# Kernel optimization log

Measured on AMD Instinct MI355X. Metric: run time of the kernel, lower is better.

The kernel has to match this reference:

```python
import jax, jax.numpy as jnp
import numpy as np


def setup_inputs() -> dict:
    key = jax.random.key(0)
    ks = jax.random.split(key, 4)
    B, C, H, W = 4, 256, 64, 64
    Cqk = C // 16
    x = jax.random.normal(ks[0], (B, C, H, W), dtype=jnp.float32)
    # 1x1 conv weights (fan-in scaled) and biases
    Wq = jax.random.normal(ks[1], (Cqk, C), dtype=jnp.float32) / np.sqrt(C)
    Wk = jax.random.normal(ks[2], (Cqk, C), dtype=jnp.float32) / np.sqrt(C)
    Wv = jax.random.normal(ks[3], (C, C), dtype=jnp.float32) / np.sqrt(C)
    bq = jnp.zeros((Cqk,), dtype=jnp.float32)
    bk = jnp.zeros((Cqk,), dtype=jnp.float32)
    bv = jnp.zeros((C,), dtype=jnp.float32)
    gamma = jnp.zeros((1,), dtype=jnp.float32)
    return {"x": x, "Wq": Wq, "bq": bq, "Wk": Wk, "bk": bk, "Wv": Wv, "bv": bv, "gamma": gamma}


def reference(x, Wq, bq, Wk, bk, Wv, bv, gamma):
    B, C, H, W = x.shape
    N = H * W
    xf = x.reshape(B, C, N)  # [B, C, N]
    # 1x1 convs == per-pixel channel matmuls
    q = jnp.einsum('oc,bcn->bon', Wq, xf) + bq[None, :, None]  # [B, C//16, N]
    k = jnp.einsum('oc,bcn->bon', Wk, xf) + bk[None, :, None]  # [B, C//16, N]
    v = jnp.einsum('oc,bcn->bon', Wv, xf) + bv[None, :, None]  # [B, C, N]
    # S = Q^T K : [B, N, N]
    S = jnp.einsum('bcn,bcm->bnm', q, k)
    # NOTE: original uses Softmax(dim=-2) -> normalize over the first N axis (query/row axis)
    A = jax.nn.softmax(S, axis=-2)
    # o[b,c,m] = sum_n v[b,c,n] * A[b,n,m]  (torch.bmm(proj_value, softmax(S)))
    o = jnp.einsum('bcn,bnm->bcm', v, A).reshape(B, C, H, W)
    return x + gamma[0] * o
```

## Files before the change

### kernel.cpp

```cpp
#include <hip/hip_runtime.h>
#include <hip/hip_bf16.h>


constexpr int B_  = 4;
constexpr int C_  = 256;
constexpr int N_  = 4096;
constexpr int NT  = 64;

typedef short   bf16x8  __attribute__((ext_vector_type(8)));
typedef short   short4v __attribute__((ext_vector_type(4)));
typedef unsigned short ushort8v __attribute__((ext_vector_type(8)));
typedef float   f32x4   __attribute__((ext_vector_type(4)));

__device__ __forceinline__ unsigned short f2bf(float f) {
  __hip_bfloat16 h = __float2bfloat16(f);
  return *reinterpret_cast<unsigned short*>(&h);
}

__global__ __launch_bounds__(256) void cast_w_kernel(
    const float* __restrict__ Wq, const float* __restrict__ Wk,
    const float* __restrict__ Wv, unsigned short* __restrict__ Wbf) {
  const int f = (blockIdx.x * 256 + threadIdx.x) * 8;
  const float* src;
  if (f < 4096)      src = Wq + f;
  else if (f < 8192) src = Wk + (f - 4096);
  else               src = Wv + (f - 8192);
  f32x4 a = *(const f32x4*)src;
  f32x4 c = *(const f32x4*)(src + 4);
  ushort8v o;
#pragma unroll
  for (int e = 0; e < 4; ++e) { o[e] = f2bf(a[e]); o[4 + e] = f2bf(c[e]); }
  *(ushort8v*)&Wbf[f] = o;
}

__global__ __launch_bounds__(512) void proj_fused_kernel(
    const float* __restrict__ x, const unsigned short* __restrict__ Wbf,
    const float* __restrict__ bq, const float* __restrict__ bk,
    const float* __restrict__ bv,
    unsigned short* __restrict__ qT, unsigned short* __restrict__ kT,
    unsigned short* __restrict__ vbf) {
  __shared__ __align__(16) char xsm[32768];
  const int tid = threadIdx.x;
  const int b  = blockIdx.y;
  const int n0 = blockIdx.x << 6;
  const int ln = tid & 63, w = tid >> 6;
  const int g  = ln >> 4, li = ln & 15;
  const float* xb = x + (size_t)b * C_ * N_ + n0;

#pragma unroll
  for (int pass = 0; pass < 2; ++pass) {
    const int id = pass * 512 + tid;
    const int nq = id & 15, kq = id >> 4;
    const int k = kq << 2, nn = nq << 2;
    f32x4 r0 = *(const f32x4*)&xb[(size_t)(k + 0) * N_ + nn];
    f32x4 r1 = *(const f32x4*)&xb[(size_t)(k + 1) * N_ + nn];
    f32x4 r2 = *(const f32x4*)&xb[(size_t)(k + 2) * N_ + nn];
    f32x4 r3 = *(const f32x4*)&xb[(size_t)(k + 3) * N_ + nn];
#pragma unroll
    for (int j = 0; j < 4; ++j) {
      short4v p;
      p[0] = (short)f2bf(r0[j]); p[1] = (short)f2bf(r1[j]);
      p[2] = (short)f2bf(r2[j]); p[3] = (short)f2bf(r3[j]);
      const int row = nn + j;
      const int boff = row * 512 + (((k >> 3) ^ (row & 7)) << 4) + ((k & 7) << 1);
      *(short4v*)(xsm + boff) = p;
    }
  }
  __syncthreads();

  const int nmf = (w < 2) ? 3 : 2;
  const int mfs0 = 2 * w, mfs1 = 2 * w + 1, mfs2 = 16 + w;
  f32x4 acc[3][4];
#pragma unroll
  for (int mi = 0; mi < 3; ++mi)
#pragma unroll
    for (int nf = 0; nf < 4; ++nf) acc[mi][nf] = (f32x4){0.f, 0.f, 0.f, 0.f};

  const char* wb = (const char*)Wbf;
#pragma unroll
  for (int kk = 0; kk < 8; ++kk) {
    bf16x8 bx[4];
#pragma unroll
    for (int nf = 0; nf < 4; ++nf) {
      const int row = nf * 16 + li;
      bx[nf] = *(const bf16x8*)(xsm + row * 512 + ((((kk << 2) + g) ^ (li & 7)) << 4));
    }
#pragma unroll
    for (int mi = 0; mi < 3; ++mi) {
      if (mi < nmf) {
        const int mf = (mi == 0) ? mfs0 : (mi == 1 ? mfs1 : mfs2);
        bf16x8 af = *(const bf16x8*)(wb + (size_t)(mf * 16 + li) * 512 + kk * 64 + g * 16);
#pragma unroll
        for (int nf = 0; nf < 4; ++nf)
          acc[mi][nf] = __builtin_amdgcn_mfma_f32_16x16x32_bf16(af, bx[nf], acc[mi][nf], 0, 0, 0);
      }
    }
  }

#pragma unroll
  for (int mi = 0; mi < 3; ++mi) {
    if (mi < nmf) {
      const int mf = (mi == 0) ? mfs0 : (mi == 1 ? mfs1 : mfs2);
      f32x4 bb;
      if (mf == 0)      bb = *(const f32x4*)&bq[4 * g];
      else if (mf == 1) bb = *(const f32x4*)&bk[4 * g];
      else              bb = *(const f32x4*)&bv[(mf - 2) * 16 + 4 * g];
      if (mf >= 2) {
        const int c = (mf - 2) * 16 + 4 * g;
        unsigned short* vout = vbf + ((size_t)b * C_ + c) * N_ + n0;
#pragma unroll
        for (int r = 0; r < 4; ++r)
#pragma unroll
          for (int nf = 0; nf < 4; ++nf)
            vout[(size_t)r * N_ + nf * 16 + li] = f2bf(acc[mi][nf][r] + bb[r]);
      } else {
        unsigned short* o = (mf == 0 ? qT : kT) + ((size_t)b * N_ + n0) * 24 + 4 * g;
#pragma unroll
        for (int nf = 0; nf < 4; ++nf)
#pragma unroll
          for (int r = 0; r < 4; ++r)
            o[(size_t)(nf * 16 + li) * 24 + r] = f2bf(acc[mi][nf][r] + bb[r]);
      }
    }
  }
}

__global__ __launch_bounds__(512) void attn_fused_kernel(
    const float* __restrict__ x, const unsigned short* __restrict__ qT,
    const unsigned short* __restrict__ kT, const unsigned short* __restrict__ vbf,
    const float* __restrict__ sgamma, float* __restrict__ out) {
  __shared__ __align__(16) char smem[33312];
  char* Pl0 = smem;
  char* Pl1 = smem + 8192;
  float* Tl   = (float*)smem;
  float* denl = (float*)(smem + 32768);

  const int tid = threadIdx.x;
  const int ln = tid & 63, w = tid >> 6;
  const int g  = ln >> 4, li = ln & 15;
  const int fmS  = w >> 1;
  const int fnS0 = (w & 1) << 1;

  const int orig = blockIdx.x;
  const int swz  = ((orig & 7) << 5) + (orig >> 3);
  const int b  = swz >> 6;
  const int m0 = (swz & 63) << 6;

  const char* qbase = (const char*)qT + (size_t)b * N_ * 48;
  const char* kbase = (const char*)kT + (size_t)b * N_ * 48;
  const char* vb    = (const char*)vbf + (size_t)b * C_ * N_ * 2;

  const bf16x8 Z8 = (bf16x8){0, 0, 0, 0, 0, 0, 0, 0};

  const bf16x8 kfrag = (g < 2)
      ? *(const bf16x8*)(kbase + (size_t)(m0 + fmS * 16 + li) * 48 + g * 16) : Z8;

  const char* qp0 = qbase + (size_t)(fnS0 * 16 + li) * 48 + g * 16;
  const char* vp0 = vb + (size_t)(w * 32 + li) * (N_ * 2) + g * 16;

  f32x4 oacc[2][4];
#pragma unroll
  for (int c2 = 0; c2 < 2; ++c2)
#pragma unroll
    for (int mf = 0; mf < 4; ++mf) oacc[c2][mf] = (f32x4){0.f, 0.f, 0.f, 0.f};
  float den_part = 0.f;

  bf16x8 qA0, qA1, qB0, qB1;
  bf16x8 vA[2][2], vB[2][2];

  qA0 = (g < 2) ? *(const bf16x8*)(qp0) : Z8;
  qA1 = (g < 2) ? *(const bf16x8*)(qp0 + 768) : Z8;
#pragma unroll
  for (int c2 = 0; c2 < 2; ++c2)
#pragma unroll
    for (int ks = 0; ks < 2; ++ks)
      vA[c2][ks] = *(const bf16x8*)(vp0 + (size_t)c2 * (16 * N_ * 2) + ks * 64);

#define TILE(CQ0, CQ1, CV, NQ0, NQ1, NV, PBUF, T) do {                               \
    const size_t tnb = (size_t)(((T) + 1) & 63);                                     \
    NQ0 = (g < 2) ? *(const bf16x8*)(qp0 + tnb * 3072) : Z8;                         \
    NQ1 = (g < 2) ? *(const bf16x8*)(qp0 + tnb * 3072 + 768) : Z8;                   \
    _Pragma("unroll")                                                                \
    for (int c2 = 0; c2 < 2; ++c2)                                                   \
      _Pragma("unroll")                                                              \
      for (int ks = 0; ks < 2; ++ks)                                                 \
        NV[c2][ks] = *(const bf16x8*)(vp0 + tnb * 128 +                              \
                                      (size_t)c2 * (16 * N_ * 2) + ks * 64);         \
    {                                 \
      const int mrow = fmS * 16 + li;                                                \
      f32x4 s0 = (f32x4){0.f, 0.f, 0.f, 0.f};                                        \
      s0 = __builtin_amdgcn_mfma_f32_16x16x32_bf16(CQ0, kfrag, s0, 0, 0, 0);         \
      float e0 = __expf(s0[0]), e1 = __expf(s0[1]);                                  \
      float e2 = __expf(s0[2]), e3 = __expf(s0[3]);                                  \
      den_part += (e0 + e1) + (e2 + e3);                                             \
      short4v pk0;                                                                   \
      pk0[0] = (short)f2bf(e0); pk0[1] = (short)f2bf(e1);                            \
      pk0[2] = (short)f2bf(e2); pk0[3] = (short)f2bf(e3);                            \
      *(short4v*)((PBUF) + mrow * 128 +                                              \
                  (((fnS0 << 5) + (g << 3)) ^ ((mrow & 7) << 4))) = pk0;             \
      f32x4 s1 = (f32x4){0.f, 0.f, 0.f, 0.f};                                        \
      s1 = __builtin_amdgcn_mfma_f32_16x16x32_bf16(CQ1, kfrag, s1, 0, 0, 0);         \
      float f0 = __expf(s1[0]), f1 = __expf(s1[1]);                                  \
      float f2v = __expf(s1[2]), f3 = __expf(s1[3]);                                 \
      den_part += (f0 + f1) + (f2v + f3);                                            \
      short4v pk1;                                                                   \
      pk1[0] = (short)f2bf(f0); pk1[1] = (short)f2bf(f1);                            \
      pk1[2] = (short)f2bf(f2v); pk1[3] = (short)f2bf(f3);                           \
      *(short4v*)((PBUF) + mrow * 128 +                                              \
                  ((((fnS0 + 1) << 5) + (g << 3)) ^ ((mrow & 7) << 4))) = pk1;       \
    }                                                                                \
    asm volatile("s_waitcnt lgkmcnt(0)" ::: "memory");                               \
    __builtin_amdgcn_sched_barrier(0);                                               \
    __builtin_amdgcn_s_barrier();                                                    \
    __builtin_amdgcn_sched_barrier(0);                                               \
    _Pragma("unroll")                                                                \
    for (int ks = 0; ks < 2; ++ks) {                                                 \
      bf16x8 bfr[4];                                                                 \
      _Pragma("unroll")                                                              \
      for (int mf = 0; mf < 4; ++mf) {                                               \
        const int mr = mf * 16 + li;                                                 \
        bfr[mf] = *(const bf16x8*)((PBUF) + mr * 128 +                               \
                                   (((ks << 6) + (g << 4)) ^ ((mr & 7) << 4)));      \
      }                                                                              \
      _Pragma("unroll")                                                              \
      for (int c2 = 0; c2 < 2; ++c2)                                                 \
        _Pragma("unroll")                                                            \
        for (int mf = 0; mf < 4; ++mf)                                               \
          oacc[c2][mf] = __builtin_amdgcn_mfma_f32_16x16x32_bf16(                    \
              CV[c2][ks], bfr[mf], oacc[c2][mf], 0, 0, 0);                           \
    }                                                                                \
  } while (0)

  for (int tt = 0; tt < NT / 2; ++tt) {
    TILE(qA0, qA1, vA, qB0, qB1, vB, Pl0, 2 * tt);
    TILE(qB0, qB1, vB, qA0, qA1, vA, Pl1, 2 * tt + 1);
  }
#undef TILE

  float d = den_part;
  d += __shfl_xor(d, 16, 64);
  d += __shfl_xor(d, 32, 64);
  if (ln < 16) denl[w * 16 + li] = d;
  __syncthreads();

  float rden[4];
#pragma unroll
  for (int mf = 0; mf < 4; ++mf)
    rden[mf] = 1.f / (denl[(2 * mf) * 16 + li] + denl[(2 * mf + 1) * 16 + li]);
  const float gam = sgamma[0];

#pragma unroll
  for (int h = 0; h < 2; ++h) {
    __syncthreads();
    if ((w >> 2) == h) {
#pragma unroll
      for (int c2 = 0; c2 < 2; ++c2)
#pragma unroll
        for (int mf = 0; mf < 4; ++mf)
#pragma unroll
          for (int r = 0; r < 4; ++r)
            Tl[((w & 3) * 32 + c2 * 16 + 4 * g + r) * 64 + mf * 16 + li] =
                oacc[c2][mf][r] * rden[mf];
    }
    __syncthreads();
#pragma unroll
    for (int p = 0; p < 4; ++p) {
      const int clocal = (p << 5) + (tid >> 4);
      const int c  = (h << 7) + clocal;
      const int mo = (tid & 15) << 2;
      const size_t gi = ((size_t)b * C_ + c) * N_ + m0 + mo;
      const float4 xa = *(const float4*)&x[gi];
      const f32x4  ov = *(const f32x4*)&Tl[clocal * 64 + mo];
      float4 rr;
      rr.x = xa.x + gam * ov[0];
      rr.y = xa.y + gam * ov[1];
      rr.z = xa.z + gam * ov[2];
      rr.w = xa.w + gam * ov[3];
      *(float4*)&out[gi] = rr;
    }
  }
}

extern "C" void kernel_launch(void* const* d_in, const int* in_sizes, int n_in,
                              void* d_out, int out_size, void* d_ws, size_t ws_size,
                              hipStream_t stream) {
  const float* x     = (const float*)d_in[0];
  const float* Wq    = (const float*)d_in[1];
  const float* bq    = (const float*)d_in[2];
  const float* Wk    = (const float*)d_in[3];
  const float* bk    = (const float*)d_in[4];
  const float* Wv    = (const float*)d_in[5];
  const float* bv    = (const float*)d_in[6];
  const float* gamma = (const float*)d_in[7];
  float* out = (float*)d_out;

  unsigned short* qTg = (unsigned short*)d_ws;
  unsigned short* kTg = qTg + (size_t)B_ * N_ * 24;
  unsigned short* vbf = kTg + (size_t)B_ * N_ * 24;
  unsigned short* Wbf = vbf + (size_t)B_ * C_ * N_;

  cast_w_kernel<<<36, 256, 0, stream>>>(Wq, Wk, Wv, Wbf);
  proj_fused_kernel<<<dim3(64, 4), 512, 0, stream>>>(x, Wbf, bq, bk, bv, qTg, kTg, vbf);
  attn_fused_kernel<<<256, 512, 0, stream>>>(x, qTg, kTg, vbf, gamma, out);
}
```

Before: 161.9 us.

## Split attention channels across blocks and restage projection through LDS

The attention kernel now splits the 256 output channels into two halves per block and launches 512 blocks, each warp covering a quarter of channels and half of the query columns. The goal is more parallelism and lower register pressure, at the cost of recomputing the softmax score tiles twice. The projection kernel now processes 128 pixels per block, with the output channels split across two blocks. It stages weights in LDS and writes results through shared memory for coalesced global stores. Setprio hints are added around the PV MFMA section.

```diff
diff --git a/kernel.cpp b/kernel.cpp
--- a/kernel.cpp
+++ b/kernel.cpp
@@ -2,10 +2,10 @@
 #include <hip/hip_bf16.h>
 
 
-constexpr int B_  = 4;
-constexpr int C_  = 256;
-constexpr int N_  = 4096;
-constexpr int NT  = 64;
+constexpr int B_ = 4;
+constexpr int C_ = 256;
+constexpr int N_ = 4096;
+constexpr int NT = 64;
 
 typedef short   bf16x8  __attribute__((ext_vector_type(8)));
 typedef short   short4v __attribute__((ext_vector_type(4)));
@@ -39,93 +39,127 @@
     const float* __restrict__ bv,
     unsigned short* __restrict__ qT, unsigned short* __restrict__ kT,
     unsigned short* __restrict__ vbf) {
-  __shared__ __align__(16) char xsm[32768];
+  __shared__ __align__(16) char smem[139264];
+  char* xsm = smem;
+  char* Wsm = smem + 65536;
   const int tid = threadIdx.x;
-  const int b  = blockIdx.y;
-  const int n0 = blockIdx.x << 6;
+  const int n0 = blockIdx.x << 7;
+  const int mh = blockIdx.y;
+  const int b  = blockIdx.z;
   const int ln = tid & 63, w = tid >> 6;
   const int g  = ln >> 4, li = ln & 15;
-  const float* xb = x + (size_t)b * C_ * N_ + n0;
-
-#pragma unroll
-  for (int pass = 0; pass < 2; ++pass) {
-    const int id = pass * 512 + tid;
-    const int nq = id & 15, kq = id >> 4;
-    const int k = kq << 2, nn = nq << 2;
-    f32x4 r0 = *(const f32x4*)&xb[(size_t)(k + 0) * N_ + nn];
-    f32x4 r1 = *(const f32x4*)&xb[(size_t)(k + 1) * N_ + nn];
-    f32x4 r2 = *(const f32x4*)&xb[(size_t)(k + 2) * N_ + nn];
-    f32x4 r3 = *(const f32x4*)&xb[(size_t)(k + 3) * N_ + nn];
-#pragma unroll
-    for (int j = 0; j < 4; ++j) {
-      short4v p;
-      p[0] = (short)f2bf(r0[j]); p[1] = (short)f2bf(r1[j]);
-      p[2] = (short)f2bf(r2[j]); p[3] = (short)f2bf(r3[j]);
-      const int row = nn + j;
-      const int boff = row * 512 + (((k >> 3) ^ (row & 7)) << 4) + ((k & 7) << 1);
-      *(short4v*)(xsm + boff) = p;
-    }
-  }
-  __syncthreads();
-
-  const int nmf = (w < 2) ? 3 : 2;
-  const int mfs0 = 2 * w, mfs1 = 2 * w + 1, mfs2 = 16 + w;
-  f32x4 acc[3][4];
-#pragma unroll
-  for (int mi = 0; mi < 3; ++mi)
-#pragma unroll
-    for (int nf = 0; nf < 4; ++nf) acc[mi][nf] = (f32x4){0.f, 0.f, 0.f, 0.f};
-
-  const char* wb = (const char*)Wbf;
+
+  {
+    const unsigned short* wsrc = Wbf + (size_t)mh * 144 * 256;
+#pragma unroll
+    for (int p = 0; p < 9; ++p) {
+      const int id = p * 512 + tid;
+      const int row = id >> 5, slot = id & 31;
+      *(f32x4*)(Wsm + row * 512 + ((slot ^ (row & 7)) << 4)) =
+          *(const f32x4*)(wsrc + row * 256 + slot * 8);
+    }
+  }
+  {
+    const float* xb = x + (size_t)b * C_ * N_ + n0;
+#pragma unroll
+    for (int pass = 0; pass < 4; ++pass) {
+      const int id = pass * 512 + tid;
+      const int nq = id & 31, kq = id >> 5;
+      const int k = kq << 2, nn = nq << 2;
+      f32x4 r0 = *(const f32x4*)&xb[(size_t)(k + 0) * N_ + nn];
+      f32x4 r1 = *(const f32x4*)&xb[(size_t)(k + 1) * N_ + nn];
+      f32x4 r2 = *(const f32x4*)&xb[(size_t)(k + 2) * N_ + nn];
+      f32x4 r3 = *(const f32x4*)&xb[(size_t)(k + 3) * N_ + nn];
+#pragma unroll
+      for (int j = 0; j < 4; ++j) {
+        short4v p;
+        p[0] = (short)f2bf(r0[j]); p[1] = (short)f2bf(r1[j]);
+        p[2] = (short)f2bf(r2[j]); p[3] = (short)f2bf(r3[j]);
+        const int row = nn + j;
+        *(short4v*)(xsm + row * 512 + (((k >> 3) ^ (row & 7)) << 4) + ((k & 7) << 1)) = p;
+      }
+    }
+  }
+  __syncthreads();
+
+  const bool two = (w == 0);
+  f32x4 acc[2][8];
+#pragma unroll
+  for (int s = 0; s < 2; ++s)
+#pragma unroll
+    for (int nf = 0; nf < 8; ++nf) acc[s][nf] = (f32x4){0.f, 0.f, 0.f, 0.f};
+
 #pragma unroll
   for (int kk = 0; kk < 8; ++kk) {
-    bf16x8 bx[4];
-#pragma unroll
-    for (int nf = 0; nf < 4; ++nf) {
-      const int row = nf * 16 + li;
-      bx[nf] = *(const bf16x8*)(xsm + row * 512 + ((((kk << 2) + g) ^ (li & 7)) << 4));
-    }
-#pragma unroll
-    for (int mi = 0; mi < 3; ++mi) {
-      if (mi < nmf) {
-        const int mf = (mi == 0) ? mfs0 : (mi == 1 ? mfs1 : mfs2);
-        bf16x8 af = *(const bf16x8*)(wb + (size_t)(mf * 16 + li) * 512 + kk * 64 + g * 16);
-#pragma unroll
-        for (int nf = 0; nf < 4; ++nf)
-          acc[mi][nf] = __builtin_amdgcn_mfma_f32_16x16x32_bf16(af, bx[nf], acc[mi][nf], 0, 0, 0);
-      }
-    }
-  }
-
-#pragma unroll
-  for (int mi = 0; mi < 3; ++mi) {
-    if (mi < nmf) {
-      const int mf = (mi == 0) ? mfs0 : (mi == 1 ? mfs1 : mfs2);
-      f32x4 bb;
-      if (mf == 0)      bb = *(const f32x4*)&bq[4 * g];
-      else if (mf == 1) bb = *(const f32x4*)&bk[4 * g];
-      else              bb = *(const f32x4*)&bv[(mf - 2) * 16 + 4 * g];
-      if (mf >= 2) {
-        const int c = (mf - 2) * 16 + 4 * g;
-        unsigned short* vout = vbf + ((size_t)b * C_ + c) * N_ + n0;
+    const int soff = ((((kk << 2) + g) ^ (li & 7)) << 4);
+    bf16x8 bx[8];
+#pragma unroll
+    for (int nf = 0; nf < 8; ++nf)
+      bx[nf] = *(const bf16x8*)(xsm + (nf * 16 + li) * 512 + soff);
+    bf16x8 a0 = *(const bf16x8*)(Wsm + (size_t)(w * 16 + li) * 512 + soff);
+#pragma unroll
+    for (int nf = 0; nf < 8; ++nf)
+      acc[0][nf] = __builtin_amdgcn_mfma_f32_16x16x32_bf16(a0, bx[nf], acc[0][nf], 0, 0, 0);
+    if (two) {
+      bf16x8 a1 = *(const bf16x8*)(Wsm + (size_t)(8 * 16 + li) * 512 + soff);
+#pragma unroll
+      for (int nf = 0; nf < 8; ++nf)
+        acc[1][nf] = __builtin_amdgcn_mfma_f32_16x16x32_bf16(a1, bx[nf], acc[1][nf], 0, 0, 0);
+    }
+  }
+  __syncthreads();
+
+  unsigned short* vsm = (unsigned short*)xsm;
+  unsigned short* qsm = (unsigned short*)(xsm + 36864);
+  unsigned short* ksm = (unsigned short*)(xsm + 40960);
+#pragma unroll
+  for (int s = 0; s < 2; ++s) {
+    if (s == 1 && !two) break;
+    const int gf = mh * 9 + (s == 0 ? w : 8);
+    f32x4 bb;
+    if (gf == 0)      bb = *(const f32x4*)&bq[4 * g];
+    else if (gf == 1) bb = *(const f32x4*)&bk[4 * g];
+    else              bb = *(const f32x4*)&bv[(gf - 2) * 16 + 4 * g];
+    if (gf >= 2) {
+      const int vb16 = (gf - 2 - mh * 7) << 4;
+#pragma unroll
+      for (int r = 0; r < 4; ++r)
+#pragma unroll
+        for (int nf = 0; nf < 8; ++nf)
+          vsm[(vb16 + 4 * g + r) * 128 + nf * 16 + li] = f2bf(acc[s][nf][r] + bb[r]);
+    } else {
+      unsigned short* t = (gf == 0) ? qsm : ksm;
+#pragma unroll
+      for (int nf = 0; nf < 8; ++nf)
 #pragma unroll
         for (int r = 0; r < 4; ++r)
-#pragma unroll
-          for (int nf = 0; nf < 4; ++nf)
-            vout[(size_t)r * N_ + nf * 16 + li] = f2bf(acc[mi][nf][r] + bb[r]);
-      } else {
-        unsigned short* o = (mf == 0 ? qT : kT) + ((size_t)b * N_ + n0) * 24 + 4 * g;
-#pragma unroll
-        for (int nf = 0; nf < 4; ++nf)
-#pragma unroll
-          for (int r = 0; r < 4; ++r)
-            o[(size_t)(nf * 16 + li) * 24 + r] = f2bf(acc[mi][nf][r] + bb[r]);
-      }
-    }
-  }
-}
-
-__global__ __launch_bounds__(512) void attn_fused_kernel(
+          t[(nf * 16 + li) * 16 + 4 * g + r] = f2bf(acc[s][nf][r] + bb[r]);
+    }
+  }
+  __syncthreads();
+
+  const int nchunk = (mh ? 144 : 112) * 16;
+#pragma unroll
+  for (int p = 0; p < 5; ++p) {
+    const int id = p * 512 + tid;
+    if (id < nchunk) {
+      const int vr = id >> 4, off = id & 15;
+      const int c = mh * 112 + vr;
+      *(f32x4*)(vbf + ((size_t)b * C_ + c) * N_ + n0 + off * 8) =
+          *(const f32x4*)(vsm + vr * 128 + off * 8);
+    }
+  }
+  if (mh == 0) {
+    const unsigned short* ssm = (tid < 256) ? qsm : ksm;
+    unsigned short* dst = (tid < 256) ? qT : kT;
+    const int t2 = tid & 255;
+    const int n = t2 >> 1, half = t2 & 1;
+    *(f32x4*)(dst + ((size_t)b * N_ + n0 + n) * 24 + half * 8) =
+        *(const f32x4*)(ssm + n * 16 + half * 8);
+  }
+}
+
+__global__ __launch_bounds__(512, 4) void attn_fused_kernel(
     const float* __restrict__ x, const unsigned short* __restrict__ qT,
     const unsigned short* __restrict__ kT, const unsigned short* __restrict__ vbf,
     const float* __restrict__ sgamma, float* __restrict__ out) {
@@ -140,11 +174,15 @@
   const int g  = ln >> 4, li = ln & 15;
   const int fmS  = w >> 1;
   const int fnS0 = (w & 1) << 1;
+  const int wcq  = w & 3;
+  const int wmh  = w >> 2;
 
   const int orig = blockIdx.x;
-  const int swz  = ((orig & 7) << 5) + (orig >> 3);
-  const int b  = swz >> 6;
-  const int m0 = (swz & 63) << 6;
+  const int L    = ((orig & 7) << 6) + (orig >> 3);
+  const int b    = L >> 7;
+  const int rem  = L & 127;
+  const int m0   = (rem >> 1) << 6;
+  const int ch   = rem & 1;
 
   const char* qbase = (const char*)qT + (size_t)b * N_ * 48;
   const char* kbase = (const char*)kT + (size_t)b * N_ * 48;
@@ -156,13 +194,13 @@
       ? *(const bf16x8*)(kbase + (size_t)(m0 + fmS * 16 + li) * 48 + g * 16) : Z8;
 
   const char* qp0 = qbase + (size_t)(fnS0 * 16 + li) * 48 + g * 16;
-  const char* vp0 = vb + (size_t)(w * 32 + li) * (N_ * 2) + g * 16;
-
-  f32x4 oacc[2][4];
-#pragma unroll
-  for (int c2 = 0; c2 < 2; ++c2)
-#pragma unroll
-    for (int mf = 0; mf < 4; ++mf) oacc[c2][mf] = (f32x4){0.f, 0.f, 0.f, 0.f};
+  const char* vp0 = vb + (size_t)(ch * 128 + wcq * 32 + li) * (N_ * 2) + g * 16;
+
+  f32x4 oacc[2][2];
+#pragma unroll
+  for (int cf = 0; cf < 2; ++cf)
+#pragma unroll
+    for (int mf = 0; mf < 2; ++mf) oacc[cf][mf] = (f32x4){0.f, 0.f, 0.f, 0.f};
   float den_part = 0.f;
 
   bf16x8 qA0, qA1, qB0, qB1;
@@ -171,21 +209,21 @@
   qA0 = (g < 2) ? *(const bf16x8*)(qp0) : Z8;
   qA1 = (g < 2) ? *(const bf16x8*)(qp0 + 768) : Z8;
 #pragma unroll
-  for (int c2 = 0; c2 < 2; ++c2)
+  for (int cf = 0; cf < 2; ++cf)
 #pragma unroll
     for (int ks = 0; ks < 2; ++ks)
-      vA[c2][ks] = *(const bf16x8*)(vp0 + (size_t)c2 * (16 * N_ * 2) + ks * 64);
+      vA[cf][ks] = *(const bf16x8*)(vp0 + (size_t)cf * (16 * N_ * 2) + ks * 64);
 
 #define TILE(CQ0, CQ1, CV, NQ0, NQ1, NV, PBUF, T) do {                               \
     const size_t tnb = (size_t)(((T) + 1) & 63);                                     \
     NQ0 = (g < 2) ? *(const bf16x8*)(qp0 + tnb * 3072) : Z8;                         \
     NQ1 = (g < 2) ? *(const bf16x8*)(qp0 + tnb * 3072 + 768) : Z8;                   \
     _Pragma("unroll")                                                                \
-    for (int c2 = 0; c2 < 2; ++c2)                                                   \
+    for (int cf = 0; cf < 2; ++cf)                                                   \
       _Pragma("unroll")                                                              \
       for (int ks = 0; ks < 2; ++ks)                                                 \
-        NV[c2][ks] = *(const bf16x8*)(vp0 + tnb * 128 +                              \
-                                      (size_t)c2 * (16 * N_ * 2) + ks * 64);         \
+        NV[cf][ks] = *(const bf16x8*)(vp0 + tnb * 128 +                              \
+                                      (size_t)cf * (16 * N_ * 2) + ks * 64);         \
     {                                 \
       const int mrow = fmS * 16 + li;                                                \
       f32x4 s0 = (f32x4){0.f, 0.f, 0.f, 0.f};                                        \
@@ -213,22 +251,24 @@
     __builtin_amdgcn_sched_barrier(0);                                               \
     __builtin_amdgcn_s_barrier();                                                    \
     __builtin_amdgcn_sched_barrier(0);                                               \
+    __builtin_amdgcn_s_setprio(1);                                                   \
     _Pragma("unroll")                                                                \
     for (int ks = 0; ks < 2; ++ks) {                                                 \
-      bf16x8 bfr[4];                                                                 \
+      bf16x8 bfr[2];                                                                 \
       _Pragma("unroll")                                                              \
-      for (int mf = 0; mf < 4; ++mf) {                                               \
-        const int mr = mf * 16 + li;                                                 \
+      for (int mf = 0; mf < 2; ++mf) {                                               \
+        const int mr = (2 * wmh + mf) * 16 + li;                                     \
         bfr[mf] = *(const bf16x8*)((PBUF) + mr * 128 +                               \
                                    (((ks << 6) + (g << 4)) ^ ((mr & 7) << 4)));      \
       }                                                                              \
       _Pragma("unroll")                                                              \
-      for (int c2 = 0; c2 < 2; ++c2)                                                 \
+      for (int cf = 0; cf < 2; ++cf)                                                 \
         _Pragma("unroll")                                                            \
-        for (int mf = 0; mf < 4; ++mf)                                               \
-          oacc[c2][mf] = __builtin_amdgcn_mfma_f32_16x16x32_bf16(                    \
-              CV[c2][ks], bfr[mf], oacc[c2][mf], 0, 0, 0);                           \
+        for (int mf = 0; mf < 2; ++mf)                                               \
+          oacc[cf][mf] = __builtin_amdgcn_mfma_f32_16x16x32_bf16(                    \
+              CV[cf][ks], bfr[mf], oacc[cf][mf], 0, 0, 0);                           \
     }                                                                                \
+    __builtin_amdgcn_s_setprio(0);                                                   \
   } while (0)
 
   for (int tt = 0; tt < NT / 2; ++tt) {
@@ -243,41 +283,36 @@
   if (ln < 16) denl[w * 16 + li] = d;
   __syncthreads();
 
-  float rden[4];
-#pragma unroll
-  for (int mf = 0; mf < 4; ++mf)
-    rden[mf] = 1.f / (denl[(2 * mf) * 16 + li] + denl[(2 * mf + 1) * 16 + li]);
+  float rden[2];
+#pragma unroll
+  for (int mf = 0; mf < 2; ++mf) {
+    const int fmg = 2 * wmh + mf;
+    rden[mf] = 1.f / (denl[(2 * fmg) * 16 + li] + denl[(2 * fmg + 1) * 16 + li]);
+  }
   const float gam = sgamma[0];
 
 #pragma unroll
-  for (int h = 0; h < 2; ++h) {
-    __syncthreads();
-    if ((w >> 2) == h) {
-#pragma unroll
-      for (int c2 = 0; c2 < 2; ++c2)
-#pragma unroll
-        for (int mf = 0; mf < 4; ++mf)
-#pragma unroll
-          for (int r = 0; r < 4; ++r)
-            Tl[((w & 3) * 32 + c2 * 16 + 4 * g + r) * 64 + mf * 16 + li] =
-                oacc[c2][mf][r] * rden[mf];
-    }
-    __syncthreads();
-#pragma unroll
-    for (int p = 0; p < 4; ++p) {
-      const int clocal = (p << 5) + (tid >> 4);
-      const int c  = (h << 7) + clocal;
-      const int mo = (tid & 15) << 2;
-      const size_t gi = ((size_t)b * C_ + c) * N_ + m0 + mo;
-      const float4 xa = *(const float4*)&x[gi];
-      const f32x4  ov = *(const f32x4*)&Tl[clocal * 64 + mo];
-      float4 rr;
-      rr.x = xa.x + gam * ov[0];
-      rr.y = xa.y + gam * ov[1];
-      rr.z = xa.z + gam * ov[2];
-      rr.w = xa.w + gam * ov[3];
-      *(float4*)&out[gi] = rr;
-    }
+  for (int cf = 0; cf < 2; ++cf)
+#pragma unroll
+    for (int mf = 0; mf < 2; ++mf)
+#pragma unroll
+      for (int r = 0; r < 4; ++r)
+        Tl[(wcq * 32 + cf * 16 + 4 * g + r) * 64 + wmh * 32 + mf * 16 + li] =
+            oacc[cf][mf][r] * rden[mf];
+  __syncthreads();
+#pragma unroll
+  for (int p = 0; p < 4; ++p) {
+    const int id = p * 512 + tid;
+    const int cl = id >> 4, mo = (id & 15) << 2;
+    const size_t gi = ((size_t)b * C_ + ch * 128 + cl) * N_ + m0 + mo;
+    const float4 xa = *(const float4*)&x[gi];
+    const f32x4  ov = *(const f32x4*)&Tl[cl * 64 + mo];
+    float4 rr;
+    rr.x = xa.x + gam * ov[0];
+    rr.y = xa.y + gam * ov[1];
+    rr.z = xa.z + gam * ov[2];
+    rr.w = xa.w + gam * ov[3];
+    *(float4*)&out[gi] = rr;
   }
 }
 
@@ -300,6 +335,6 @@
   unsigned short* Wbf = vbf + (size_t)B_ * C_ * N_;
 
   cast_w_kernel<<<36, 256, 0, stream>>>(Wq, Wk, Wv, Wbf);
-  proj_fused_kernel<<<dim3(64, 4), 512, 0, stream>>>(x, Wbf, bq, bk, bv, qTg, kTg, vbf);
-  attn_fused_kernel<<<256, 512, 0, stream>>>(x, qTg, kTg, vbf, gamma, out);
-}
+  proj_fused_kernel<<<dim3(32, 2, 4), 512, 0, stream>>>(x, Wbf, bq, bk, bv, qTg, kTg, vbf);
+  attn_fused_kernel<<<512, 512, 0, stream>>>(x, qTg, kTg, vbf, gamma, out);
+}
```

After: 220.7 us. 1.36x slower.

## Split projection kernel into output-channel thirds and stage outputs through LDS

Applied to the files above, without the earlier changes.

The projection kernel now launches three blocks per 64-pixel tile, each computing 96 of the 288 output rows (q, k and v channels) with 256 threads. That triples the grid from 256 to 768 blocks for better CU occupancy. Results are written to shared memory first and then stored to global memory as coalesced 16-byte vectors, replacing scattered 2-byte stores. The cost is that every block reloads and re-converts the full x tile, so x is read three times.

```diff
diff --git a/kernel.cpp b/kernel.cpp
--- a/kernel.cpp
+++ b/kernel.cpp
@@ -2,10 +2,10 @@
 #include <hip/hip_bf16.h>
 
 
-constexpr int B_  = 4;
-constexpr int C_  = 256;
-constexpr int N_  = 4096;
-constexpr int NT  = 64;
+constexpr int B_ = 4;
+constexpr int C_ = 256;
+constexpr int N_ = 4096;
+constexpr int NT = 64;
 
 typedef short   bf16x8  __attribute__((ext_vector_type(8)));
 typedef short   short4v __attribute__((ext_vector_type(4)));
@@ -33,95 +33,102 @@
   *(ushort8v*)&Wbf[f] = o;
 }
 
-__global__ __launch_bounds__(512) void proj_fused_kernel(
+__global__ __launch_bounds__(256) void proj_fused_kernel(
     const float* __restrict__ x, const unsigned short* __restrict__ Wbf,
     const float* __restrict__ bq, const float* __restrict__ bk,
     const float* __restrict__ bv,
     unsigned short* __restrict__ qT, unsigned short* __restrict__ kT,
     unsigned short* __restrict__ vbf) {
-  __shared__ __align__(16) char xsm[32768];
+  __shared__ __align__(16) char smem[32768];
   const int tid = threadIdx.x;
-  const int b  = blockIdx.y;
-  const int n0 = blockIdx.x << 6;
+  const int n0    = blockIdx.x << 6;
+  const int third = blockIdx.y;
+  const int b     = blockIdx.z;
   const int ln = tid & 63, w = tid >> 6;
   const int g  = ln >> 4, li = ln & 15;
-  const float* xb = x + (size_t)b * C_ * N_ + n0;
-
-#pragma unroll
-  for (int pass = 0; pass < 2; ++pass) {
-    const int id = pass * 512 + tid;
-    const int nq = id & 15, kq = id >> 4;
-    const int k = kq << 2, nn = nq << 2;
-    f32x4 r0 = *(const f32x4*)&xb[(size_t)(k + 0) * N_ + nn];
-    f32x4 r1 = *(const f32x4*)&xb[(size_t)(k + 1) * N_ + nn];
-    f32x4 r2 = *(const f32x4*)&xb[(size_t)(k + 2) * N_ + nn];
-    f32x4 r3 = *(const f32x4*)&xb[(size_t)(k + 3) * N_ + nn];
-#pragma unroll
-    for (int j = 0; j < 4; ++j) {
-      short4v p;
-      p[0] = (short)f2bf(r0[j]); p[1] = (short)f2bf(r1[j]);
-      p[2] = (short)f2bf(r2[j]); p[3] = (short)f2bf(r3[j]);
-      const int row = nn + j;
-      const int boff = row * 512 + (((k >> 3) ^ (row & 7)) << 4) + ((k & 7) << 1);
-      *(short4v*)(xsm + boff) = p;
+
+  {
+    const float* xb = x + (size_t)b * C_ * N_ + n0;
+#pragma unroll
+    for (int pass = 0; pass < 4; ++pass) {
+      const int id = pass * 256 + tid;
+      const int nq = id & 15, kq = id >> 4;
+      const int k = kq << 2, nn = nq << 2;
+      f32x4 r0 = *(const f32x4*)&xb[(size_t)(k + 0) * N_ + nn];
+      f32x4 r1 = *(const f32x4*)&xb[(size_t)(k + 1) * N_ + nn];
+      f32x4 r2 = *(const f32x4*)&xb[(size_t)(k + 2) * N_ + nn];
+      f32x4 r3 = *(const f32x4*)&xb[(size_t)(k + 3) * N_ + nn];
+#pragma unroll
+      for (int j = 0; j < 4; ++j) {
+        short4v p;
+        p[0] = (short)f2bf(r0[j]); p[1] = (short)f2bf(r1[j]);
+        p[2] = (short)f2bf(r2[j]); p[3] = (short)f2bf(r3[j]);
+        const int row = nn + j;
+        *(short4v*)(smem + row * 512 + (((k >> 3) ^ (row & 7)) << 4) + ((k & 7) << 1)) = p;
+      }
     }
   }
   __syncthreads();
 
-  const int nmf = (w < 2) ? 3 : 2;
-  const int mfs0 = 2 * w, mfs1 = 2 * w + 1, mfs2 = 16 + w;
-  f32x4 acc[3][4];
-#pragma unroll
-  for (int mi = 0; mi < 3; ++mi)
-#pragma unroll
-    for (int nf = 0; nf < 4; ++nf) acc[mi][nf] = (f32x4){0.f, 0.f, 0.f, 0.f};
-
-  const char* wb = (const char*)Wbf;
+  f32x4 acc[6];
+#pragma unroll
+  for (int mf = 0; mf < 6; ++mf) acc[mf] = (f32x4){0.f, 0.f, 0.f, 0.f};
+  const char* wb = (const char*)Wbf + (size_t)third * 96 * 512;
 #pragma unroll
   for (int kk = 0; kk < 8; ++kk) {
-    bf16x8 bx[4];
-#pragma unroll
-    for (int nf = 0; nf < 4; ++nf) {
-      const int row = nf * 16 + li;
-      bx[nf] = *(const bf16x8*)(xsm + row * 512 + ((((kk << 2) + g) ^ (li & 7)) << 4));
-    }
-#pragma unroll
-    for (int mi = 0; mi < 3; ++mi) {
-      if (mi < nmf) {
-        const int mf = (mi == 0) ? mfs0 : (mi == 1 ? mfs1 : mfs2);
-        bf16x8 af = *(const bf16x8*)(wb + (size_t)(mf * 16 + li) * 512 + kk * 64 + g * 16);
-#pragma unroll
-        for (int nf = 0; nf < 4; ++nf)
-          acc[mi][nf] = __builtin_amdgcn_mfma_f32_16x16x32_bf16(af, bx[nf], acc[mi][nf], 0, 0, 0);
-      }
-    }
-  }
-
-#pragma unroll
-  for (int mi = 0; mi < 3; ++mi) {
-    if (mi < nmf) {
-      const int mf = (mi == 0) ? mfs0 : (mi == 1 ? mfs1 : mfs2);
-      f32x4 bb;
-      if (mf == 0)      bb = *(const f32x4*)&bq[4 * g];
-      else if (mf == 1) bb = *(const f32x4*)&bk[4 * g];
-      else              bb = *(const f32x4*)&bv[(mf - 2) * 16 + 4 * g];
-      if (mf >= 2) {
-        const int c = (mf - 2) * 16 + 4 * g;
-        unsigned short* vout = vbf + ((size_t)b * C_ + c) * N_ + n0;
-#pragma unroll
-        for (int r = 0; r < 4; ++r)
-#pragma unroll
-          for (int nf = 0; nf < 4; ++nf)
-            vout[(size_t)r * N_ + nf * 16 + li] = f2bf(acc[mi][nf][r] + bb[r]);
-      } else {
-        unsigned short* o = (mf == 0 ? qT : kT) + ((size_t)b * N_ + n0) * 24 + 4 * g;
-#pragma unroll
-        for (int nf = 0; nf < 4; ++nf)
-#pragma unroll
-          for (int r = 0; r < 4; ++r)
-            o[(size_t)(nf * 16 + li) * 24 + r] = f2bf(acc[mi][nf][r] + bb[r]);
-      }
-    }
+    const int soff = ((((kk << 2) + g) ^ (li & 7)) << 4);
+    bf16x8 bx = *(const bf16x8*)(smem + (w * 16 + li) * 512 + soff);
+#pragma unroll
+    for (int mf = 0; mf < 6; ++mf) {
+      bf16x8 af = *(const bf16x8*)(wb + (size_t)(mf * 16 + li) * 512 + kk * 64 + g * 16);
+      acc[mf] = __builtin_amdgcn_mfma_f32_16x16x32_bf16(af, bx, acc[mf], 0, 0, 0);
+    }
+  }
+  __syncthreads();
+
+  unsigned short* vsm = (unsigned short*)smem;
+  unsigned short* qsm = (unsigned short*)(smem + 12288);
+  unsigned short* ksm = (unsigned short*)(smem + 14336);
+#pragma unroll
+  for (int mf = 0; mf < 6; ++mf) {
+    const int gf = third * 6 + mf;
+    f32x4 bb;
+    if (gf == 0)      bb = *(const f32x4*)&bq[4 * g];
+    else if (gf == 1) bb = *(const f32x4*)&bk[4 * g];
+    else              bb = *(const f32x4*)&bv[(gf - 2) * 16 + 4 * g];
+    if (gf >= 2) {
+      const int cL = (third == 0 ? (mf - 2) : mf) << 4;
+#pragma unroll
+      for (int r = 0; r < 4; ++r)
+        vsm[(cL + 4 * g + r) * 64 + w * 16 + li] = f2bf(acc[mf][r] + bb[r]);
+    } else {
+      unsigned short* t = (gf == 0) ? qsm : ksm;
+#pragma unroll
+      for (int r = 0; r < 4; ++r)
+        t[(w * 16 + li) * 16 + 4 * g + r] = f2bf(acc[mf][r] + bb[r]);
+    }
+  }
+  __syncthreads();
+
+  const int vrows = (third == 0) ? 64 : 96;
+  const int c0    = (third == 0) ? 0 : (third == 1 ? 64 : 160);
+  const int nch   = vrows * 8;
+#pragma unroll
+  for (int p = 0; p < 3; ++p) {
+    const int id = p * 256 + tid;
+    if (id < nch) {
+      const int vr = id >> 3, off = id & 7;
+      *(f32x4*)(vbf + ((size_t)b * C_ + c0 + vr) * N_ + n0 + off * 8) =
+          *(const f32x4*)(vsm + vr * 64 + off * 8);
+    }
+  }
+  if (third == 0) {
+    const unsigned short* ssm = (tid < 128) ? qsm : ksm;
+    unsigned short* dst = (tid < 128) ? qT : kT;
+    const int t2 = tid & 127;
+    const int n = t2 >> 1, half = t2 & 1;
+    *(f32x4*)(dst + ((size_t)b * N_ + n0 + n) * 24 + half * 8) =
+        *(const f32x4*)(ssm + n * 16 + half * 8);
   }
 }
 
@@ -300,6 +307,6 @@
   unsigned short* Wbf = vbf + (size_t)B_ * C_ * N_;
 
   cast_w_kernel<<<36, 256, 0, stream>>>(Wq, Wk, Wv, Wbf);
-  proj_fused_kernel<<<dim3(64, 4), 512, 0, stream>>>(x, Wbf, bq, bk, bv, qTg, kTg, vbf);
+  proj_fused_kernel<<<dim3(64, 3, 4), 256, 0, stream>>>(x, Wbf, bq, bk, bv, qTg, kTg, vbf);
   attn_fused_kernel<<<256, 512, 0, stream>>>(x, qTg, kTg, vbf, gamma, out);
 }
```

Result: slower. 174.6 us (+7.8%).
